# Kernel tuning notes

Hardware: AMD Instinct MI355X
Metric: run time of the kernel (lower is better)

The kernel has to match this reference:

```python
import jax, jax.numpy as jnp
import numpy as np

# Module configuration (from init_kwargs)
N, C_IN, C_OUT, L, V, P = 4, 64, 64, 1024, 25, 3
KERNEL_SIZE, STRIDE = 9, 1
EPS = 1e-5


def _toeplitz(length):
    # Faithful to: sum_i pad(eye(L - stride*i), (i*stride, 0, 0, i*stride))
    # -> ones at [r, r + i*stride] for i in range(kernel_size // stride)
    t = jnp.zeros((length, length), dtype=jnp.float32)
    for i in range(KERNEL_SIZE // STRIDE):  # small fixed loop over taps
        t = t + jnp.eye(length, k=i * STRIDE, dtype=jnp.float32)
    return t


def setup_inputs() -> dict:
    key = jax.random.key(0)
    k0, k1, k2, k3 = jax.random.split(key, 4)
    x = jax.random.normal(k0, (N, C_IN, L, V), dtype=jnp.float32)
    A = jax.random.uniform(k1, (P, V, V), dtype=jnp.float32)
    edge_importance = jnp.ones((P, V, V), dtype=jnp.float32)
    conv_w = jax.random.normal(k2, (C_OUT * P, C_IN, 1, 1), dtype=jnp.float32) * 0.05
    conv_b = jax.random.normal(k3, (C_OUT * P,), dtype=jnp.float32) * 0.05
    gamma = jnp.ones((C_OUT,), dtype=jnp.float32)
    beta = jnp.zeros((C_OUT,), dtype=jnp.float32)
    return {"x": x, "A": A, "edge_importance": edge_importance,
            "conv_w": conv_w, "conv_b": conv_b, "gamma": gamma, "beta": beta}


def reference(x, A, edge_importance, conv_w, conv_b, gamma, beta):
    n, _, l, v = x.shape
    res = x  # residual: in_channels == out_channels and stride == 1 -> identity

    # 1x1 conv: (N, C_in, L, V) -> (N, P*C_out, L, V)
    w = conv_w[:, :, 0, 0]  # (P*C_out, C_in)
    y = jnp.einsum('nclv,kc->nklv', x, w) + conv_b[None, :, None, None]

    # split into P chunks of C_out along channels, stack, permute -> (N, L, P, C_out, V)
    y = y.reshape(n, P, C_OUT, l, v).transpose(0, 3, 1, 2, 4)

    # partition-wise graph adjacency matmul with edge-importance mask
    y = jnp.einsum('nlpcv,pvw->nlpcw', y, A * edge_importance)

    # Toeplitz temporal conv: (N, P, C, V, L) @ (L, L)
    y = y.transpose(0, 2, 3, 4, 1)
    y = jnp.matmul(y, _toeplitz(l))
    y = y.sum(axis=1)            # sum over partitions -> (N, C, V, L)
    y = y.transpose(0, 1, 3, 2)  # (N, C, L, V)

    # BatchNorm2d with batch statistics (track_running_stats=False) + ReLU
    mean = y.mean(axis=(0, 2, 3), keepdims=True)
    var = y.var(axis=(0, 2, 3), keepdims=True)  # biased, as torch uses for normalization
    y = (y - mean) * jax.lax.rsqrt(var + EPS)
    y = y * gamma[None, :, None, None] + beta[None, :, None, None]
    y = jax.nn.relu(y)

    # do = Sequential(ReLU, Dropout(0.0)) applied to (y + res)
    return jax.nn.relu(y + res)
```

## Files before the change

kernel.cpp:

```cpp
#include <hip/hip_runtime.h>


typedef unsigned short ushort_t;
typedef __attribute__((ext_vector_type(8))) short short8;
typedef __attribute__((ext_vector_type(4))) float f32x4;
typedef __attribute__((ext_vector_type(4))) unsigned short us4;
typedef __attribute__((ext_vector_type(8))) unsigned short us8;

#define N_  4
#define CI_ 64
#define CO_ 64
#define L_  1024
#define V_  25
#define P_  3
#define KS_ 9
#define NLV 102400.0f
#define NREP 128

__device__ __forceinline__ float b2f(ushort_t u) {
  union { float f; unsigned int i; } c; c.i = ((unsigned int)u) << 16; return c.f;
}
__device__ __forceinline__ ushort_t f2b(float f) {
  union { float f; unsigned int i; } c; c.f = f;
  unsigned int u = c.i;
  u += 0x7fffu + ((u >> 16) & 1u);
  return (ushort_t)(u >> 16);
}

__global__ __launch_bounds__(256) void kwin(
    const float* __restrict__ x, ushort_t* __restrict__ xs,
    const float* __restrict__ A, const float* __restrict__ E,
    const float* __restrict__ cb, const float* __restrict__ W,
    ushort_t* __restrict__ a2raw, float* __restrict__ biastab,
    ushort_t* __restrict__ wb, float* __restrict__ statsbuf)
{
  const int chunk = blockIdx.x;
  const int n = blockIdx.y;
  const int tid = threadIdx.x;

  if (chunk == 128) {
    if (n != 0) return;
    __shared__ float colA[P_ * 32];
    if (tid < P_ * 32) {
      int p = tid >> 5, w = tid & 31;
      float s = 0.f;
      if (w < V_)
        for (int v = 0; v < V_; ++v) {
          int idx = (p * V_ + v) * V_ + w;
          s += A[idx] * E[idx];
        }
      colA[tid] = s;
    }
    for (int e = tid; e < 32 * 96; e += 256) {
      int w = e / 96, k = e - w * 96;
      int p = k >> 5, v = k & 31;
      float val = 0.f;
      if (w < V_ && v < V_) {
        int idx = (p * V_ + v) * V_ + w;
        val = A[idx] * E[idx];
      }
      a2raw[e] = f2b(val);
    }
    for (int e = tid; e < 192 * 64; e += 256) wb[e] = f2b(W[e]);
    __syncthreads();
    for (int e = tid; e < 32 * 64; e += 256) {
      int w = e >> 6, c = e & 63;
      float s = 0.f;
      for (int p = 0; p < P_; ++p) s += cb[p * 64 + c] * colA[p * 32 + w];
      biastab[e] = s;
    }
    for (int e = tid; e < NREP * 128; e += 256) statsbuf[e] = 0.f;
    return;
  }

  __shared__ ushort_t tile[64 * 402];
  const int l0 = chunk * 8;
  const long xn = (long)n * CI_ * L_ * V_;
  for (int m = tid; m < 6400; m += 256) {
    int ci = m / 100;
    int j4 = (m - ci * 100) * 4;
    f32x4 d;
    if (chunk == 0 && j4 < 200) {
      d = (f32x4){0.f, 0.f, 0.f, 0.f};
    } else {
      d = *(const f32x4*)(x + xn + (long)ci * (L_ * V_) + (l0 - 8) * V_ + j4);
    }
    ushort_t* dst = &tile[ci * 402 + j4];
    dst[0] = f2b(d[0]); dst[1] = f2b(d[1]); dst[2] = f2b(d[2]); dst[3] = f2b(d[3]);
  }
  __syncthreads();
  const long xsbase = ((long)n * L_ + l0) * 1600;
  for (int cid = tid; cid < 1600; cid += 256) {
    const int v = cid >> 6, ci = cid & 63;
    const ushort_t* col = &tile[ci * 402 + v];
    float s = 0.f;
#pragma unroll
    for (int li = 0; li < 9; ++li) s += b2f(col[li * 25]);
    xs[xsbase + cid] = f2b(s);
#pragma unroll
    for (int l_ = 1; l_ < 8; ++l_) {
      s += b2f(col[(l_ + 8) * 25]) - b2f(col[(l_ - 1) * 25]);
      xs[xsbase + l_ * 1600 + cid] = f2b(s);
    }
  }
}

__global__ __launch_bounds__(256, 4) void kmain(
    const ushort_t* __restrict__ xs,
    const ushort_t* __restrict__ Wb,
    const ushort_t* __restrict__ a2,
    const float*    __restrict__ biastab,
    ushort_t*       __restrict__ zb,
    float*          __restrict__ statsbuf)
{
  const int lb = blockIdx.x;
  const int n  = blockIdx.y;
  const int tid = threadIdx.x, lane = tid & 63, wv = tid >> 6;
  const int m16 = lane & 15, quad = lane >> 4;

  __shared__ __align__(16) ushort_t T1[13312];

  short8 af[3][2];
#pragma unroll
  for (int i = 0; i < 3; ++i) {
    const ushort_t* wrow = Wb + ((wv * 3 + i) * 16 + m16) * 64 + quad * 8;
    af[i][0] = *(const short8*)(wrow);
    af[i][1] = *(const short8*)(wrow + 32);
  }

  const ushort_t* xsb = xs + ((long)n * L_ + 4 * lb) * 1600;
  const int cbase = wv * 16 + quad * 4;
  float s1[4] = {0.f, 0.f, 0.f, 0.f}, s2[4] = {0.f, 0.f, 0.f, 0.f};

#pragma unroll
  for (int pair = 0; pair < 2; ++pair) {
    short8 bfr[4][2];
#pragma unroll
    for (int nt = 0; nt < 4; ++nt) {
      const int v = (nt & 1) * 16 + m16;
      const int l_ = pair * 2 + (nt >> 1);
#pragma unroll
      for (int ks = 0; ks < 2; ++ks) {
        short8 t = (short8){0, 0, 0, 0, 0, 0, 0, 0};
        if (v < V_)
          t = *(const short8*)(xsb + l_ * 1600 + v * 64 + ks * 32 + quad * 8);
        bfr[nt][ks] = t;
      }
    }

    f32x4 acc1[3][4];
#pragma unroll
    for (int i = 0; i < 3; ++i)
#pragma unroll
      for (int j = 0; j < 4; ++j) acc1[i][j] = (f32x4){0.f, 0.f, 0.f, 0.f};

#pragma unroll
    for (int i = 0; i < 3; ++i)
#pragma unroll
      for (int nt = 0; nt < 4; ++nt) {
        acc1[i][nt] = __builtin_amdgcn_mfma_f32_16x16x32_bf16(af[i][0], bfr[nt][0], acc1[i][nt], 0, 0, 0);
        acc1[i][nt] = __builtin_amdgcn_mfma_f32_16x16x32_bf16(af[i][1], bfr[nt][1], acc1[i][nt], 0, 0, 0);
      }

    if (pair) __syncthreads();
#pragma unroll
    for (int i = 0; i < 3; ++i) {
      const int mt = wv * 3 + i;
#pragma unroll
      for (int nt = 0; nt < 4; ++nt) {
        const int l_ = nt >> 1;
        const int col = (nt & 1) * 16 + m16;
#pragma unroll
        for (int r = 0; r < 4; ++r) {
          int k = mt * 16 + quad * 4 + r;
          T1[l_ * 6656 + (k & 63) * 104 + (k >> 6) * 32 + col] = f2b(acc1[i][nt][r]);
        }
      }
    }
    __syncthreads();

    short8 bfr2[2][3];
#pragma unroll
    for (int nt = 0; nt < 2; ++nt)
#pragma unroll
      for (int ks = 0; ks < 3; ++ks)
        bfr2[nt][ks] = *(const short8*)(a2 + (nt * 16 + m16) * 96 + ks * 32 + quad * 8);

    f32x4 acc2[2][2];
#pragma unroll
    for (int l_ = 0; l_ < 2; ++l_)
#pragma unroll
      for (int nt = 0; nt < 2; ++nt) acc2[l_][nt] = (f32x4){0.f, 0.f, 0.f, 0.f};

#pragma unroll
    for (int l_ = 0; l_ < 2; ++l_)
#pragma unroll
      for (int ks = 0; ks < 3; ++ks) {
        short8 afT = *(const short8*)(&T1[l_ * 6656 + (wv * 16 + m16) * 104 + ks * 32 + quad * 8]);
        acc2[l_][0] = __builtin_amdgcn_mfma_f32_16x16x32_bf16(afT, bfr2[0][ks], acc2[l_][0], 0, 0, 0);
        acc2[l_][1] = __builtin_amdgcn_mfma_f32_16x16x32_bf16(afT, bfr2[1][ks], acc2[l_][1], 0, 0, 0);
      }

#pragma unroll
    for (int l_ = 0; l_ < 2; ++l_) {
      const int l = 4 * lb + pair * 2 + l_;
      const float cnt = (float)(l + 1 < KS_ ? l + 1 : KS_);
#pragma unroll
      for (int nt = 0; nt < 2; ++nt) {
        const int w = nt * 16 + m16;
        if (w < V_) {
          f32x4 bias = *(const f32x4*)(biastab + w * 64 + cbase);
          us4 pack;
#pragma unroll
          for (int r = 0; r < 4; ++r) {
            pack[r] = f2b(acc2[l_][nt][r] + cnt * bias[r]);
            float zr = b2f(pack[r]);
            s1[r] += zr; s2[r] += zr * zr;
          }
          *(us4*)(&zb[(((long)(n * L_ + l) * V_ + w) << 6) + cbase]) = pack;
        }
      }
    }
  }
#pragma unroll
  for (int off = 1; off < 16; off <<= 1) {
#pragma unroll
    for (int r = 0; r < 4; ++r) {
      s1[r] += __shfl_xor(s1[r], off, 64);
      s2[r] += __shfl_xor(s2[r], off, 64);
    }
  }
  if (m16 == 0) {
    float* sb = statsbuf + ((n * 256 + lb) & (NREP - 1)) * 128;
#pragma unroll
    for (int r = 0; r < 4; ++r) {
      atomicAdd(&sb[cbase + r], s1[r]);
      atomicAdd(&sb[64 + cbase + r], s2[r]);
    }
  }
}

__global__ __launch_bounds__(256) void kapply(
    const ushort_t* __restrict__ zb, const float* __restrict__ x,
    const float* __restrict__ statsbuf,
    const float* __restrict__ gamma, const float* __restrict__ beta,
    float* __restrict__ out)
{
  const int n = blockIdx.y, chunk = blockIdx.x;
  const int tid = threadIdx.x;
  __shared__ ushort_t zl[200 * 66];
  __shared__ float red[4][64][2];
  __shared__ float sc[64], sh[64];
  const long zbase = (long)((n * L_ + chunk * 8) * V_) * 64;
  for (int m = tid; m < 6400; m += 256) {
    *(unsigned int*)(&zl[(m >> 5) * 66 + (m & 31) * 2]) =
        ((const unsigned int*)(zb + zbase))[m];
  }
  {
    const int c = tid & 63, grp = tid >> 6;
    float a = 0.f, b = 0.f;
    for (int k = grp; k < NREP; k += 4) {
      a += statsbuf[k * 128 + c];
      b += statsbuf[k * 128 + 64 + c];
    }
    red[grp][c][0] = a;
    red[grp][c][1] = b;
  }
  __syncthreads();
  if (tid < 64) {
    const float inv = 1.0f / NLV;
    float s  = red[0][tid][0] + red[1][tid][0] + red[2][tid][0] + red[3][tid][0];
    float sq = red[0][tid][1] + red[1][tid][1] + red[2][tid][1] + red[3][tid][1];
    float mean = s * inv;
    float var  = sq * inv - mean * mean;
    float rstd = rsqrtf(var + 1e-5f);
    float g = gamma[tid];
    sc[tid] = rstd * g;
    sh[tid] = beta[tid] - mean * rstd * g;
  }
  __syncthreads();
  const long obase = ((long)(n * 64) * L_ + chunk * 8) * V_;
  for (int m = tid; m < 3200; m += 256) {
    int c = m / 50, q = m - c * 50, rr = q * 4;
    long xi = obase + (long)c * (L_ * V_) + rr;
    f32x4 xv = *(const f32x4*)(x + xi);
    f32x4 o;
#pragma unroll
    for (int j = 0; j < 4; ++j) {
      float z = b2f(zl[(rr + j) * 66 + c]);
      float y = fmaxf(z * sc[c] + sh[c], 0.f);
      o[j] = fmaxf(y + xv[j], 0.f);
    }
    *(f32x4*)(out + xi) = o;
  }
}

extern "C" void kernel_launch(void* const* d_in, const int* in_sizes, int n_in,
                              void* d_out, int out_size, void* d_ws, size_t ws_size,
                              hipStream_t stream)
{
  const float* x     = (const float*)d_in[0];
  const float* A     = (const float*)d_in[1];
  const float* E     = (const float*)d_in[2];
  const float* W     = (const float*)d_in[3];
  const float* cb    = (const float*)d_in[4];
  const float* gamma = (const float*)d_in[5];
  const float* beta  = (const float*)d_in[6];
  float* out = (float*)d_out;

  char* ws = (char*)d_ws;
  const size_t XS_OFF   = 0;
  const size_t ZB_OFF   = 13107200;
  const size_t WB_OFF   = 26214400;
  const size_t A2_OFF   = WB_OFF + 32768;
  const size_t BIAS_OFF = A2_OFF + 16384;
  const size_t STAT_OFF = BIAS_OFF + 16384;
  ushort_t* xs       = (ushort_t*)(ws + XS_OFF);
  ushort_t* zb       = (ushort_t*)(ws + ZB_OFF);
  ushort_t* wb       = (ushort_t*)(ws + WB_OFF);
  ushort_t* a2       = (ushort_t*)(ws + A2_OFF);
  float*    biastab  = (float*)(ws + BIAS_OFF);
  float*    statsbuf = (float*)(ws + STAT_OFF);

  kwin  <<<dim3(129, N_), 256, 0, stream>>>(x, xs, A, E, cb, W, a2, biastab, wb,
                                            statsbuf);
  kmain <<<dim3(256, N_), 256, 0, stream>>>(xs, wb, a2, biastab, zb, statsbuf);
  kapply<<<dim3(128, N_), 256, 0, stream>>>(zb, x, statsbuf, gamma, beta, out);
}
```

Measured before the change: 135.1 us.

## Fuse BN apply into main kernel via cooperative grid sync

Turns the main kernel into a cooperative launch that keeps its bf16 outputs in registers, grid-syncs, has one block reduce the batch statistics into scale and shift, grid-syncs again, and then writes the normalized, residual-added output directly. This removes the zb round trip through global memory and the separate apply kernel launch. The cost is two grid-wide barriers, a serial statistics reduction in a single block, and output writes strided by channel plane that may coalesce less well than the old apply kernel. If the occupancy check or cooperative launch fails, it falls back to the old two-kernel path.

```diff
diff --git a/kernel.cpp b/kernel.cpp
--- a/kernel.cpp
+++ b/kernel.cpp
@@ -1,4 +1,7 @@
 #include <hip/hip_runtime.h>
+#include <hip/hip_cooperative_groups.h>
+
+namespace cg = cooperative_groups;
 
 
 typedef unsigned short ushort_t;
@@ -105,13 +108,19 @@
   }
 }
 
+template<bool COOP>
 __global__ __launch_bounds__(256, 4) void kmain(
     const ushort_t* __restrict__ xs,
     const ushort_t* __restrict__ Wb,
     const ushort_t* __restrict__ a2,
     const float*    __restrict__ biastab,
     ushort_t*       __restrict__ zb,
-    float*          __restrict__ statsbuf)
+    float*          __restrict__ statsbuf,
+    float*          __restrict__ sc_sh,
+    const float*    __restrict__ gamma,
+    const float*    __restrict__ beta,
+    const float*    __restrict__ x,
+    float*          __restrict__ out)
 {
   const int lb = blockIdx.x;
   const int n  = blockIdx.y;
@@ -131,6 +140,7 @@
   const ushort_t* xsb = xs + ((long)n * L_ + 4 * lb) * 1600;
   const int cbase = wv * 16 + quad * 4;
   float s1[4] = {0.f, 0.f, 0.f, 0.f}, s2[4] = {0.f, 0.f, 0.f, 0.f};
+  us4 zpack[2][2][2];
 
 #pragma unroll
   for (int pair = 0; pair < 2; ++pair) {
@@ -217,7 +227,10 @@
             float zr = b2f(pack[r]);
             s1[r] += zr; s2[r] += zr * zr;
           }
-          *(us4*)(&zb[(((long)(n * L_ + l) * V_ + w) << 6) + cbase]) = pack;
+          if constexpr (COOP)
+            zpack[pair][l_][nt] = pack;
+          else
+            *(us4*)(&zb[(((long)(n * L_ + l) * V_ + w) << 6) + cbase]) = pack;
         }
       }
     }
@@ -237,6 +250,67 @@
       atomicAdd(&sb[cbase + r], s1[r]);
       atomicAdd(&sb[64 + cbase + r], s2[r]);
     }
+  }
+
+  if constexpr (COOP) {
+    cg::this_grid().sync();
+
+    if (lb == 0 && n == 0) {
+      float* part = (float*)T1;
+      const int slot = tid & 127, half = tid >> 7;
+      float a = 0.f;
+      for (int k = half; k < NREP; k += 2)
+        a += __hip_atomic_load(&statsbuf[k * 128 + slot],
+                               __ATOMIC_RELAXED, __HIP_MEMORY_SCOPE_AGENT);
+      part[tid] = a;
+      __syncthreads();
+      if (tid < 64) {
+        const float inv = 1.0f / NLV;
+        float s    = part[tid]      + part[128 + tid];
+        float sq   = part[64 + tid] + part[192 + tid];
+        float mean = s * inv;
+        float var  = sq * inv - mean * mean;
+        float rstd = rsqrtf(var + 1e-5f);
+        float g = gamma[tid];
+        __hip_atomic_store(&sc_sh[tid], rstd * g,
+                           __ATOMIC_RELEASE, __HIP_MEMORY_SCOPE_AGENT);
+        __hip_atomic_store(&sc_sh[64 + tid], beta[tid] - mean * rstd * g,
+                           __ATOMIC_RELEASE, __HIP_MEMORY_SCOPE_AGENT);
+      }
+    }
+
+    cg::this_grid().sync();
+
+    float sc4[4], sh4[4];
+#pragma unroll
+    for (int r = 0; r < 4; ++r) {
+      sc4[r] = __hip_atomic_load(&sc_sh[cbase + r],
+                                 __ATOMIC_ACQUIRE, __HIP_MEMORY_SCOPE_AGENT);
+      sh4[r] = __hip_atomic_load(&sc_sh[64 + cbase + r],
+                                 __ATOMIC_ACQUIRE, __HIP_MEMORY_SCOPE_AGENT);
+    }
+
+    const long cplane = (long)(L_ * V_);
+#pragma unroll
+    for (int pair = 0; pair < 2; ++pair)
+#pragma unroll
+      for (int l_ = 0; l_ < 2; ++l_) {
+        const int l = 4 * lb + pair * 2 + l_;
+#pragma unroll
+        for (int nt = 0; nt < 2; ++nt) {
+          const int w = nt * 16 + m16;
+          if (w < V_) {
+            const long base = ((long)(n * 64 + cbase)) * cplane + l * V_ + w;
+            const us4 pk = zpack[pair][l_][nt];
+#pragma unroll
+            for (int r = 0; r < 4; ++r) {
+              const long xi = base + (long)r * cplane;
+              float y = fmaxf(b2f(pk[r]) * sc4[r] + sh4[r], 0.f);
+              out[xi] = fmaxf(y + x[xi], 0.f);
+            }
+          }
+        }
+      }
   }
 }
 
@@ -315,15 +389,34 @@
   const size_t A2_OFF   = WB_OFF + 32768;
   const size_t BIAS_OFF = A2_OFF + 16384;
   const size_t STAT_OFF = BIAS_OFF + 16384;
+  const size_t SCSH_OFF = STAT_OFF + 65536;
   ushort_t* xs       = (ushort_t*)(ws + XS_OFF);
   ushort_t* zb       = (ushort_t*)(ws + ZB_OFF);
   ushort_t* wb       = (ushort_t*)(ws + WB_OFF);
   ushort_t* a2       = (ushort_t*)(ws + A2_OFF);
   float*    biastab  = (float*)(ws + BIAS_OFF);
   float*    statsbuf = (float*)(ws + STAT_OFF);
-
-  kwin  <<<dim3(129, N_), 256, 0, stream>>>(x, xs, A, E, cb, W, a2, biastab, wb,
-                                            statsbuf);
-  kmain <<<dim3(256, N_), 256, 0, stream>>>(xs, wb, a2, biastab, zb, statsbuf);
-  kapply<<<dim3(128, N_), 256, 0, stream>>>(zb, x, statsbuf, gamma, beta, out);
-}
+  float*    sc_sh    = (float*)(ws + SCSH_OFF);
+
+  kwin<<<dim3(129, N_), 256, 0, stream>>>(x, xs, A, E, cb, W, a2, biastab, wb,
+                                          statsbuf);
+
+  auto kcoop = kmain<true>;
+  int maxb = 0;
+  hipError_t qe = hipOccupancyMaxActiveBlocksPerMultiprocessor(&maxb, kcoop, 256, 0);
+  bool coop = (qe == hipSuccess) && (maxb >= 4);
+
+  if (coop) {
+    void* args[] = {&xs, &wb, &a2, &biastab, &zb, &statsbuf, &sc_sh,
+                    (void*)&gamma, (void*)&beta, (void*)&x, &out};
+    hipError_t le = hipLaunchCooperativeKernel((const void*)kcoop,
+                                               dim3(256, N_), dim3(256),
+                                               args, 0, stream);
+    if (le != hipSuccess) coop = false;
+  }
+  if (!coop) {
+    kmain<false><<<dim3(256, N_), 256, 0, stream>>>(
+        xs, wb, a2, biastab, zb, statsbuf, sc_sh, gamma, beta, x, out);
+    kapply<<<dim3(128, N_), 256, 0, stream>>>(zb, x, statsbuf, gamma, beta, out);
+  }
+}
```

New measurement: 136.3 us. No clear change (+0.9%).
